# Kernel optimization log

Hardware: AMD Instinct MI355X
Metric: run time of the kernel (lower is better)

The kernel has to match this reference:

```python
import jax, jax.numpy as jnp
import numpy as np

B, S, H = 2, 2048, 2048
NK, NV, DK, DV = 16, 32, 128, 128
K_CONV = 4
EPS = 1e-6
KEY_DIM = NK * DK          # 2048
VALUE_DIM = NV * DV        # 4096
CONV_DIM = 2 * KEY_DIM + VALUE_DIM  # 8192
R = NV // NK               # GQA repeat factor


def setup_inputs() -> dict:
    key = jax.random.key(0)
    ks = jax.random.split(key, 9)
    s = lambda d: 1.0 / np.sqrt(d)
    x = jax.random.normal(ks[0], (B, S, H), jnp.float32)
    W_qkvz = jax.random.normal(ks[1], (H, 2 * KEY_DIM + 2 * VALUE_DIM), jnp.float32) * s(H)
    W_ba = jax.random.normal(ks[2], (H, 2 * NV), jnp.float32) * s(H)
    conv_w = jax.random.normal(ks[3], (CONV_DIM, K_CONV), jnp.float32) * s(K_CONV)
    dt_bias = jnp.ones((NV,), jnp.float32)
    A_log = jnp.log(jax.random.uniform(ks[4], (NV,), jnp.float32, 1e-3, 16.0))
    norm_w = jnp.ones((DV,), jnp.float32)
    W_out = jax.random.normal(ks[5], (VALUE_DIM, H), jnp.float32) * s(VALUE_DIM)
    return {"x": x, "W_qkvz": W_qkvz, "W_ba": W_ba, "conv_w": conv_w,
            "dt_bias": dt_bias, "A_log": A_log, "norm_w": norm_w, "W_out": W_out}


def _rms_norm(x, eps=EPS):
    return x * jax.lax.rsqrt(jnp.mean(jnp.square(x), -1, keepdims=True) + eps)


def _forward(x, W_qkvz, W_ba, conv_w, dt_bias, A_log, norm_w, W_out):
    b_, s_ = x.shape[:2]
    # in projections (mlx split-INDEX semantics)
    qkvz = (x @ W_qkvz).reshape(b_, s_, NK, 2 * DK + 2 * R * DV)
    q, k, v, z = jnp.split(qkvz, [DK, 2 * DK, 2 * DK + R * DV], axis=-1)
    v = v.reshape(b_, s_, NV, DV)
    z = z.reshape(b_, s_, NV, DV)
    ba = (x @ W_ba).reshape(b_, s_, NK, 2 * R)
    b_gate, a_gate = jnp.split(ba, [R], axis=-1)
    b_gate = b_gate.reshape(b_, s_, NV)
    a_gate = a_gate.reshape(b_, s_, NV)

    # causal depthwise conv over [q,k,v] channels, zero initial conv state
    mixed = jnp.concatenate([q.reshape(b_, s_, -1), k.reshape(b_, s_, -1),
                             v.reshape(b_, s_, -1)], axis=-1)  # [B,S,CONV_DIM]
    xc = jnp.pad(mixed, ((0, 0), (K_CONV - 1, 0), (0, 0))).transpose(0, 2, 1)  # [B,C,S+K-1]
    conv = jax.lax.conv_general_dilated(
        xc, conv_w[:, None, :], window_strides=(1,), padding='VALID',
        dimension_numbers=('NCH', 'OIH', 'NCH'), feature_group_count=CONV_DIM)
    conv = jax.nn.silu(conv).transpose(0, 2, 1)  # [B,S,CONV_DIM]
    q, k, v = jnp.split(conv, [KEY_DIM, 2 * KEY_DIM], axis=-1)
    q = q.reshape(b_, s_, NK, DK)
    k = k.reshape(b_, s_, NK, DK)
    v = v.reshape(b_, s_, NV, DV)

    inv_scale = DK ** -0.5
    q = (inv_scale ** 2) * _rms_norm(q)
    k = inv_scale * _rms_norm(k)
    # GQA: repeat k/q heads to match value heads
    q = jnp.repeat(q, R, axis=2)  # [B,S,NV,DK]
    k = jnp.repeat(k, R, axis=2)

    beta = jax.nn.sigmoid(b_gate)                                # [B,S,NV]
    g = -jnp.exp(A_log) * jax.nn.softplus(a_gate + dt_bias)      # [B,S,NV] (log-decay)

    # gated delta-rule recurrence, scan over time
    def step(Sst, inp):
        q_t, k_t, v_t, g_t, beta_t = inp   # [B,NV,DK], [B,NV,DV], [B,NV]
        Sst = Sst * jnp.exp(g_t)[..., None, None]
        kv = jnp.einsum('bhk,bhkv->bhv', k_t, Sst)
        delta = (v_t - kv) * beta_t[..., None]
        Sst = Sst + k_t[..., None] * delta[:, :, None, :]
        o = jnp.einsum('bhk,bhkv->bhv', q_t, Sst)
        return Sst, o

    S0 = jnp.zeros((b_, NV, DK, DV), x.dtype)
    xs = (q.transpose(1, 0, 2, 3), k.transpose(1, 0, 2, 3), v.transpose(1, 0, 2, 3),
          g.transpose(1, 0, 2), beta.transpose(1, 0, 2))
    _, out = jax.lax.scan(step, S0, xs)
    out = out.transpose(1, 0, 2, 3)  # [B,S,NV,DV]

    # gated RMSNorm (precise swiglu)
    xn = _rms_norm(out) * norm_w
    gated = jax.nn.silu(z.astype(jnp.float32)) * xn.astype(jnp.float32)
    gated = gated.astype(x.dtype)
    return gated.reshape(b_, s_, VALUE_DIM) @ W_out


def reference(x, W_qkvz, W_ba, conv_w, dt_bias, A_log, norm_w, W_out):
    return _forward(x, W_qkvz, W_ba, conv_w, dt_bias, A_log, norm_w, W_out)
```

## Files before the change

kernel.cpp:

```cpp
#include <hip/hip_runtime.h>
#include <stdint.h>

#define B_    2
#define SEQ   2048
#define HID   2048
#define NK_   16
#define NV_   32
#define DK_   128
#define DV_   128
#define NQKVZ 12288
#define CONVD 8192
#define MTOT  (B_*SEQ)
#define CCH   16
#define HTOK  1024

typedef unsigned short ushort_t;
typedef __bf16 bf16x8 __attribute__((ext_vector_type(8)));
typedef float  f32x4  __attribute__((ext_vector_type(4)));
typedef unsigned short us4 __attribute__((ext_vector_type(4)));

__device__ __forceinline__ ushort_t f2bf(float f){
  union { float f; unsigned u; } v; v.f = f;
  unsigned r = v.u + 0x7FFFu + ((v.u >> 16) & 1u);
  return (ushort_t)(r >> 16);
}
__device__ __forceinline__ float bf2f(ushort_t u){
  union { unsigned u; float f; } v; v.u = ((unsigned)u) << 16; return v.f;
}
__device__ __forceinline__ float sigmoidf_(float x){ return 1.f/(1.f+__expf(-x)); }
__device__ __forceinline__ float siluf_(float x){ return x*sigmoidf_(x); }

__global__ void cast_x_kernel(const float* __restrict__ x, ushort_t* __restrict__ xb, int n4){
  int i = blockIdx.x*256 + threadIdx.x;
  if (i >= n4) return;
  float4 v = ((const float4*)x)[i];
  us4 o; o[0]=f2bf(v.x); o[1]=f2bf(v.y); o[2]=f2bf(v.z); o[3]=f2bf(v.w);
  ((us4*)xb)[i] = o;
}

__global__ __launch_bounds__(256) void transpose_cast(const float* __restrict__ W, ushort_t* __restrict__ Wt,
                                                      int K, int N){
  __shared__ float tile[64][65];
  int n0 = blockIdx.x*64, k0 = blockIdx.y*64;
  int tx = threadIdx.x & 63, ty = threadIdx.x >> 6;
  #pragma unroll
  for (int i=0;i<16;i++){
    int kr = ty + i*4;
    tile[kr][tx] = W[(size_t)(k0+kr)*N + n0+tx];
  }
  __syncthreads();
  #pragma unroll
  for (int i=0;i<16;i++){
    int nr = ty + i*4;
    Wt[(size_t)(n0+nr)*K + k0+tx] = f2bf(tile[tx][nr]);
  }
}

template<int OUTBF>
__global__ __launch_bounds__(512, 2) void gemm_big(const ushort_t* __restrict__ A, const ushort_t* __restrict__ Bt,
                                                   void* __restrict__ Cv, int M, int N, int K){
  extern __shared__ ushort_t dynlds[];
  ushort_t* SA = dynlds;
  ushort_t* SB = dynlds + 3*8192;
  const int t = threadIdx.x;
  const int lane = t & 63, w = t >> 6;
  const int wm = w >> 2, wn = w & 3;
  const int lr = lane & 15, hk = lane >> 4;
  const int gx = gridDim.x;
  const int nwg = gx * gridDim.y;
  const int flat = blockIdx.y*gx + blockIdx.x;
  const int cpx = nwg >> 3;
  const int swzb = (flat & 7)*cpx + (flat >> 3);
  const int m0 = (swzb / gx) * 256, n0 = (swzb % gx) * 256;

  int srow[2], scol[2];
  #pragma unroll
  for (int q=0;q<2;q++){
    int p  = (w*2+q)*1024 + lane*16;
    int lg = p ^ (((p>>9)&1)<<5);
    srow[q] = lg >> 6;
    scol[q] = (lg & 63) >> 1;
  }
  int phA[8], phB[4];
  #pragma unroll
  for (int mi=0;mi<8;mi++){
    int lg = (wm*128 + mi*16 + lr)*64 + hk*16;
    phA[mi] = lg ^ (((lg>>9)&1)<<5);
  }
  #pragma unroll
  for (int ni=0;ni<4;ni++){
    int lg = (wn*64 + ni*16 + lr)*64 + hk*16;
    phB[ni] = lg ^ (((lg>>9)&1)<<5);
  }

  auto stage = [&](int j, int bufb){
    #pragma unroll
    for (int q=0;q<2;q++)
      __builtin_amdgcn_global_load_lds(
        (const __attribute__((address_space(1))) void*)(A + (size_t)(m0+srow[q])*K + j*32 + scol[q]),
        (__attribute__((address_space(3))) void*)(SA + bufb*8192 + (w*2+q)*512), 16, 0, 0);
    #pragma unroll
    for (int q=0;q<2;q++)
      __builtin_amdgcn_global_load_lds(
        (const __attribute__((address_space(1))) void*)(Bt + (size_t)(n0+srow[q])*K + j*32 + scol[q]),
        (__attribute__((address_space(3))) void*)(SB + bufb*8192 + (w*2+q)*512), 16, 0, 0);
  };

  f32x4 acc[8][4];
  #pragma unroll
  for (int mi=0;mi<8;mi++)
    #pragma unroll
    for (int ni=0;ni<4;ni++) acc[mi][ni] = (f32x4){0.f,0.f,0.f,0.f};

  const int NT = K >> 5;
  stage(0, 0);
  stage(1, 1);
  asm volatile("s_waitcnt vmcnt(4)" ::: "memory");
  __builtin_amdgcn_s_barrier();
  __builtin_amdgcn_sched_barrier(0);

  int cur = 0;
  for (int j = 0; j < NT; ++j){
    int nb = cur + 2; if (nb >= 3) nb -= 3;
    if (j + 2 < NT) stage(j+2, nb);
    const char* bA = (const char*)(SA + cur*8192);
    const char* bB = (const char*)(SB + cur*8192);
    bf16x8 af[8], bfv[4];
    #pragma unroll
    for (int mi=0;mi<8;mi++) af[mi]  = *(const bf16x8*)(bA + phA[mi]);
    #pragma unroll
    for (int ni=0;ni<4;ni++) bfv[ni] = *(const bf16x8*)(bB + phB[ni]);
    #pragma unroll
    for (int mi=0;mi<8;mi++)
      #pragma unroll
      for (int ni=0;ni<4;ni++)
        acc[mi][ni] = __builtin_amdgcn_mfma_f32_16x16x32_bf16(af[mi], bfv[ni], acc[mi][ni], 0, 0, 0);
    if (j + 2 < NT){
      asm volatile("s_waitcnt vmcnt(4)" ::: "memory");
      __builtin_amdgcn_s_barrier();
      __builtin_amdgcn_sched_barrier(0);
    } else if (j + 1 < NT){
      asm volatile("s_waitcnt vmcnt(0)" ::: "memory");
      __builtin_amdgcn_s_barrier();
      __builtin_amdgcn_sched_barrier(0);
    }
    cur = cur + 1; if (cur >= 3) cur -= 3;
  }

  #pragma unroll
  for (int mi=0;mi<8;mi++)
    #pragma unroll
    for (int ni=0;ni<4;ni++)
      #pragma unroll
      for (int r=0;r<4;r++){
        int m = m0 + wm*128 + mi*16 + hk*4 + r;
        int n = n0 + wn*64  + ni*16 + lr;
        if (OUTBF) ((ushort_t*)Cv)[(size_t)m*N + n] = f2bf(acc[mi][ni][r]);
        else       ((float*)Cv)[(size_t)m*N + n]    = acc[mi][ni][r];
      }
}

template<int OUTBF>
__global__ __launch_bounds__(512, 2) void gemm_big2(const ushort_t* __restrict__ A, const ushort_t* __restrict__ Bt,
                                                    void* __restrict__ Cv, int M, int N, int K){
  extern __shared__ ushort_t dynlds[];
  ushort_t* SA = dynlds;
  ushort_t* SB = dynlds + 3*8192;
  const int t = threadIdx.x;
  const int lane = t & 63, w = t >> 6;
  const int wm = w >> 1, wn = w & 1;
  const int lr = lane & 15, hk = lane >> 4;
  const int gx = gridDim.x;
  const int nwg = gx * gridDim.y;
  const int flat = blockIdx.y*gx + blockIdx.x;
  const int cpx = nwg >> 3;
  const int swzb = (flat & 7)*cpx + (flat >> 3);
  const int m0 = (swzb / gx) * 256, n0 = (swzb % gx) * 128;

  int srA[2], scA[2];
  #pragma unroll
  for (int q=0;q<2;q++){
    int p  = (w*2+q)*1024 + lane*16;
    int lg = p ^ (((p>>9)&1)<<5);
    srA[q] = lg >> 6;
    scA[q] = (lg & 63) >> 1;
  }
  int srB, scB;
  {
    int p  = w*1024 + lane*16;
    int lg = p ^ (((p>>9)&1)<<5);
    srB = lg >> 6;
    scB = (lg & 63) >> 1;
  }
  int phA[4], phB[4];
  #pragma unroll
  for (int mi=0;mi<4;mi++){
    int lg = (wm*64 + mi*16 + lr)*64 + hk*16;
    phA[mi] = lg ^ (((lg>>9)&1)<<5);
  }
  #pragma unroll
  for (int ni=0;ni<4;ni++){
    int lg = (wn*64 + ni*16 + lr)*64 + hk*16;
    phB[ni] = lg ^ (((lg>>9)&1)<<5);
  }

  auto stage = [&](int j, int bufb){
    #pragma unroll
    for (int q=0;q<2;q++)
      __builtin_amdgcn_global_load_lds(
        (const __attribute__((address_space(1))) void*)(A + (size_t)(m0+srA[q])*K + j*32 + scA[q]),
        (__attribute__((address_space(3))) void*)(SA + bufb*8192 + (w*2+q)*512), 16, 0, 0);
    __builtin_amdgcn_global_load_lds(
        (const __attribute__((address_space(1))) void*)(Bt + (size_t)(n0+srB)*K + j*32 + scB),
        (__attribute__((address_space(3))) void*)(SB + bufb*4096 + w*512), 16, 0, 0);
  };

  f32x4 acc[4][4];
  #pragma unroll
  for (int mi=0;mi<4;mi++)
    #pragma unroll
    for (int ni=0;ni<4;ni++) acc[mi][ni] = (f32x4){0.f,0.f,0.f,0.f};

  const int NT = K >> 5;
  stage(0, 0);
  stage(1, 1);
  asm volatile("s_waitcnt vmcnt(3)" ::: "memory");
  __builtin_amdgcn_s_barrier();
  __builtin_amdgcn_sched_barrier(0);

  int cur = 0;
  for (int j = 0; j < NT; ++j){
    int nb = cur + 2; if (nb >= 3) nb -= 3;
    if (j + 2 < NT) stage(j+2, nb);
    const char* bA = (const char*)(SA + cur*8192);
    const char* bB = (const char*)(SB + cur*4096);
    bf16x8 af[4], bfv[4];
    #pragma unroll
    for (int mi=0;mi<4;mi++) af[mi]  = *(const bf16x8*)(bA + phA[mi]);
    #pragma unroll
    for (int ni=0;ni<4;ni++) bfv[ni] = *(const bf16x8*)(bB + phB[ni]);
    #pragma unroll
    for (int mi=0;mi<4;mi++)
      #pragma unroll
      for (int ni=0;ni<4;ni++)
        acc[mi][ni] = __builtin_amdgcn_mfma_f32_16x16x32_bf16(af[mi], bfv[ni], acc[mi][ni], 0, 0, 0);
    if (j + 2 < NT){
      asm volatile("s_waitcnt vmcnt(3)" ::: "memory");
      __builtin_amdgcn_s_barrier();
      __builtin_amdgcn_sched_barrier(0);
    } else if (j + 1 < NT){
      asm volatile("s_waitcnt vmcnt(0)" ::: "memory");
      __builtin_amdgcn_s_barrier();
      __builtin_amdgcn_sched_barrier(0);
    }
    cur = cur + 1; if (cur >= 3) cur -= 3;
  }

  #pragma unroll
  for (int mi=0;mi<4;mi++)
    #pragma unroll
    for (int ni=0;ni<4;ni++)
      #pragma unroll
      for (int r=0;r<4;r++){
        int m = m0 + wm*64 + mi*16 + hk*4 + r;
        int n = n0 + wn*64 + ni*16 + lr;
        if (OUTBF) ((ushort_t*)Cv)[(size_t)m*N + n] = f2bf(acc[mi][ni][r]);
        else       ((float*)Cv)[(size_t)m*N + n]    = acc[mi][ni][r];
      }
}

template<int OUTBF>
__global__ __launch_bounds__(256) void gemm_bf16(const ushort_t* __restrict__ A, const ushort_t* __restrict__ Bt,
                                                 void* __restrict__ Cv, int M, int N, int K){
  __shared__ ushort_t As[128][32];
  __shared__ ushort_t Bs[128][32];
  const int t = threadIdx.x;
  const int lane = t & 63, w = t >> 6;
  const int wm = w >> 1, wn = w & 1;
  const int gx = gridDim.x;
  const int nwg = gx * gridDim.y;
  const int flat = blockIdx.y*gx + blockIdx.x;
  const int cpx = nwg >> 3;
  const int swz = (flat & 7)*cpx + (flat >> 3);
  const int m0 = (swz / gx) * 128, n0 = (swz % gx) * 128;
  const int srow = lane >> 2;
  const int scol = (lane & 3) * 8;
  const ushort_t* gA0 = &A [(size_t)(m0 +      w*16 + srow)*K + scol];
  const ushort_t* gA1 = &A [(size_t)(m0 + 64 + w*16 + srow)*K + scol];
  const ushort_t* gB0 = &Bt[(size_t)(n0 +      w*16 + srow)*K + scol];
  const ushort_t* gB1 = &Bt[(size_t)(n0 + 64 + w*16 + srow)*K + scol];
  ushort_t* lA0 = &As[     w*16][0];
  ushort_t* lA1 = &As[64 + w*16][0];
  ushort_t* lB0 = &Bs[     w*16][0];
  ushort_t* lB1 = &Bs[64 + w*16][0];
  f32x4 acc[4][4];
  #pragma unroll
  for (int i=0;i<4;i++)
    #pragma unroll
    for (int j=0;j<4;j++) acc[i][j] = (f32x4){0.f,0.f,0.f,0.f};
  const int lr = lane & 15, lk = (lane >> 4) * 8;
  for (int k0 = 0; k0 < K; k0 += 32){
    __builtin_amdgcn_global_load_lds((const __attribute__((address_space(1))) void*)(gA0 + k0),
                                     (__attribute__((address_space(3))) void*)lA0, 16, 0, 0);
    __builtin_amdgcn_global_load_lds((const __attribute__((address_space(1))) void*)(gA1 + k0),
                                     (__attribute__((address_space(3))) void*)lA1, 16, 0, 0);
    __builtin_amdgcn_global_load_lds((const __attribute__((address_space(1))) void*)(gB0 + k0),
                                     (__attribute__((address_space(3))) void*)lB0, 16, 0, 0);
    __builtin_amdgcn_global_load_lds((const __attribute__((address_space(1))) void*)(gB1 + k0),
                                     (__attribute__((address_space(3))) void*)lB1, 16, 0, 0);
    __syncthreads();
    bf16x8 af[4], bfv[4];
    #pragma unroll
    for (int i=0;i<4;i++) af[i]  = *(const bf16x8*)&As[wm*64 + i*16 + lr][lk];
    #pragma unroll
    for (int j=0;j<4;j++) bfv[j] = *(const bf16x8*)&Bs[wn*64 + j*16 + lr][lk];
    #pragma unroll
    for (int i=0;i<4;i++)
      #pragma unroll
      for (int j=0;j<4;j++)
        acc[i][j] = __builtin_amdgcn_mfma_f32_16x16x32_bf16(af[i], bfv[j], acc[i][j], 0, 0, 0);
    __syncthreads();
  }
  const int lg = lane >> 4;
  #pragma unroll
  for (int i=0;i<4;i++)
    #pragma unroll
    for (int j=0;j<4;j++)
      #pragma unroll
      for (int r=0;r<4;r++){
        int m = m0 + wm*64 + i*16 + lg*4 + r;
        int n = n0 + wn*64 + j*16 + lr;
        if (OUTBF) ((ushort_t*)Cv)[(size_t)m*N + n] = f2bf(acc[i][j][r]);
        else       ((float*)Cv)[(size_t)m*N + n]    = acc[i][j][r];
      }
}

__global__ __launch_bounds__(256) void gemm_ba(const float* __restrict__ x, const float* __restrict__ Wba,
                                               float* __restrict__ ba){
  int lane = threadIdx.x & 63;
  int wid  = threadIdx.x >> 6;
  int row  = blockIdx.x*4 + wid;
  const float* xr = x + (size_t)row*HID;
  float acc = 0.f;
  for (int k=0;k<HID;k+=4){
    float4 xv = *(const float4*)&xr[k];
    acc += xv.x * Wba[(size_t)(k+0)*64 + lane];
    acc += xv.y * Wba[(size_t)(k+1)*64 + lane];
    acc += xv.z * Wba[(size_t)(k+2)*64 + lane];
    acc += xv.w * Wba[(size_t)(k+3)*64 + lane];
  }
  ba[(size_t)row*64 + lane] = acc;
}

__global__ __launch_bounds__(256) void conv_norm_kernel(const ushort_t* __restrict__ qkvz, const float* __restrict__ conv_w,
                                                        ushort_t* __restrict__ qkv){
  const int blk = blockIdx.x;
  const int bt = blk >> 4;
  const int ts = bt & (SEQ-1);
  const int gi = (blk & 15)*4 + (threadIdx.x >> 6);
  const int e2 = threadIdx.x & 63;
  const int dk = 2*e2;
  int col;
  if (gi < 16)       col = gi*768 + dk;
  else if (gi < 32)  col = (gi-16)*768 + 128 + dk;
  else { int nv = gi-32; col = (nv>>1)*768 + 256 + (nv&1)*128 + dk; }
  const int c = gi*128 + dk;
  const float4 w0 = *(const float4*)&conv_w[(size_t)c*4];
  const float4 w1 = *(const float4*)&conv_w[(size_t)(c+1)*4];
  ushort2 a0 = (ts>=3) ? *(const ushort2*)&qkvz[(size_t)(bt-3)*NQKVZ + col] : make_ushort2(0,0);
  ushort2 a1 = (ts>=2) ? *(const ushort2*)&qkvz[(size_t)(bt-2)*NQKVZ + col] : make_ushort2(0,0);
  ushort2 a2 = (ts>=1) ? *(const ushort2*)&qkvz[(size_t)(bt-1)*NQKVZ + col] : make_ushort2(0,0);
  ushort2 a3 =           *(const ushort2*)&qkvz[(size_t)(bt  )*NQKVZ + col];
  float y0 = siluf_(bf2f(a0.x)*w0.x + bf2f(a1.x)*w0.y + bf2f(a2.x)*w0.z + bf2f(a3.x)*w0.w);
  float y1 = siluf_(bf2f(a0.y)*w1.x + bf2f(a1.y)*w1.y + bf2f(a2.y)*w1.z + bf2f(a3.y)*w1.w);
  float o0 = y0, o1 = y1;
  if (gi < 32){
    float ss = y0*y0 + y1*y1;
    #pragma unroll
    for (int o=1;o<64;o<<=1) ss += __shfl_xor(ss, o);
    float rs = rsqrtf(ss*(1.f/128.f) + 1e-6f);
    float scale = (gi < 16) ? (1.f/128.f) : 0.08838834764831845f;
    o0 = y0*rs*scale; o1 = y1*rs*scale;
  }
  ushort2 ov; ov.x = f2bf(o0); ov.y = f2bf(o1);
  *(ushort2*)&qkv[(size_t)bt*CONVD + gi*128 + dk] = ov;
}

__global__ void gbeta_kernel(const float* __restrict__ ba, const float* __restrict__ A_log,
                             const float* __restrict__ dt_bias, float2* __restrict__ egb){
  int idx = blockIdx.x*256 + threadIdx.x;
  if (idx >= MTOT*NV_) return;
  int nv = idx & 31;
  int bt = idx >> 5;
  int nk = nv >> 1, r = nv & 1;
  float bg = ba[(size_t)bt*64 + nk*4 + r];
  float ag = ba[(size_t)bt*64 + nk*4 + 2 + r];
  float ad = ag + dt_bias[nv];
  float sp = fmaxf(ad, 0.f) + log1pf(__expf(-fabsf(ad)));
  float g  = -__expf(A_log[nv]) * sp;
  egb[idx] = make_float2(g, sigmoidf_(bg));
}

__global__ __launch_bounds__(512) void recurrence_chunked(const ushort_t* __restrict__ qkv,
                                                          const float2* __restrict__ egb,
                                                          float* __restrict__ outc,
                                                          ushort_t* __restrict__ oaug,
                                                          ushort_t* __restrict__ Sfin,
                                                          int pmode){
  const int bi = blockIdx.x;
  int role, hb, tokbase, ntok;
  if (pmode == 0){ role = 0; hb = bi; tokbase = 0; ntok = SEQ; }
  else { role = bi >> 7; hb = bi & 127; tokbase = (role == 0) ? 0 : HTOK; ntok = HTOK; }
  const bool isaug = (role == 2);
  const bool wsf   = (pmode == 1) && (role == 0);
  const int b    = hb >> 6;
  const int nv   = (hb >> 1) & 31;
  const int half = hb & 1;
  const int nk   = nv >> 1;
  const int t    = threadIdx.x;
  const int lane = t & 63, w = t >> 6;
  const int lr   = lane & 15, hk = lane >> 4;

  __shared__ ushort_t Kl[16*136];
  __shared__ ushort_t S0h[64*136];
  __shared__ ushort_t S0l[64*136];
  __shared__ ushort_t KT[128*40];
  __shared__ ushort_t DT[64*40];
  __shared__ ushort_t Wl[16*40];
  __shared__ float    Al[16*20];
  __shared__ float    Ul[64*20];
  __shared__ float    clB[2][16], blB[2][16], eclB[2][16], kslB[2][16], c15B[2];

  for (int i = t; i < 64*40;  i += 512) DT[i] = 0;
  for (int i = t; i < 128*40; i += 512) KT[i] = 0;
  for (int i = t; i < 16*40;  i += 512) Wl[i] = 0;
  for (int i = t; i < 64*136; i += 512){ S0h[i] = 0; S0l[i] = 0; }

  const int dt  = w >> 1;
  const int dkb = (w & 1) * 4;
  const int ot  = w - 4;
  const int st  = t >> 5, sdk = (t & 31) * 4;
  const size_t bt0 = (size_t)b*SEQ + tokbase;
  const int mytile = (w < 4) ? w : (w - 4);

  f32x4 S[4];
  #pragma unroll
  for (int tt=0;tt<4;tt++)
    #pragma unroll
    for (int r=0;r<4;r++)
      S[tt][r] = (isaug && ((dkb+tt)*16 + hk*4 + r) == (half*64 + dt*16 + lr)) ? 1.f : 0.f;

  if (isaug){
    __syncthreads();
    if (t < 64) S0h[t*136 + half*64 + t] = (ushort_t)0x3F80;
  }

  uint2 kreg = *(const uint2*)(qkv + (bt0+st)*CONVD + 2048 + nk*128 + sdk);
  bf16x8 qf[4];
  if (w >= 4){
    const ushort_t* qrow = qkv + (bt0+lr)*CONVD + nk*128 + hk*8;
    #pragma unroll
    for (int ks=0;ks<4;ks++) qf[ks] = *(const bf16x8*)(qrow + ks*32);
  }
  ushort_t vreg[4] = {0,0,0,0};
  if (w < 4 && !isaug){
    #pragma unroll
    for (int r=0;r<4;r++)
      vreg[r] = qkv[(bt0+hk*4+r)*CONVD + 4096 + nv*128 + half*64 + w*16 + lr];
  }
  {
    float2 gb = make_float2(0.f,0.f);
    if (w==1 && lane<16) gb = egb[(bt0+lane)*NV_ + nv];
    *(uint2*)&Kl[st*136 + sdk] = kreg;
    if (w==1 && lane<16){
      float c = gb.x;
      #pragma unroll
      for (int o=1;o<16;o<<=1){ float tv = __shfl_up(c, o, 16); if (lane >= o) c += tv; }
      clB[0][lane] = c; blB[0][lane] = gb.y; eclB[0][lane] = __expf(c);
      float c15 = __shfl(c, 15, 16);
      kslB[0][lane] = __expf(c15 - c);
      if (lane==0) c15B[0] = c15;
    }
  }
  __syncthreads();

  int pb = 0;
  for (int base = 0; base < ntok; base += CCH){
    const int nbase = (base + CCH < ntok) ? base + CCH : base;

    bf16x8 kf[4];
    if (w <= 4){
      #pragma unroll
      for (int ks=0;ks<4;ks++) kf[ks] = *(const bf16x8*)&Kl[lr*136 + hk*8 + ks*32];
    }
    f32x4 ph = (f32x4){0.f,0.f,0.f,0.f}, pl = ph;
    __builtin_amdgcn_s_setprio(1);
    #pragma unroll
    for (int ks=0;ks<4;ks++){
      bf16x8 xf = (w < 4) ? kf[ks] : qf[ks];
      bf16x8 yh = *(const bf16x8*)&S0h[(mytile*16+lr)*136 + hk*8 + ks*32];
      bf16x8 yl = *(const bf16x8*)&S0l[(mytile*16+lr)*136 + hk*8 + ks*32];
      ph = __builtin_amdgcn_mfma_f32_16x16x32_bf16(xf, yh, ph, 0,0,0);
      pl = __builtin_amdgcn_mfma_f32_16x16x32_bf16(xf, yl, pl, 0,0,0);
    }
    __builtin_amdgcn_s_setprio(0);
    if (w == 1){
      f32x4 a = (f32x4){0.f,0.f,0.f,0.f};
      #pragma unroll
      for (int ks=0;ks<4;ks++) a = __builtin_amdgcn_mfma_f32_16x16x32_bf16(kf[ks], kf[ks], a, 0,0,0);
      #pragma unroll
      for (int r=0;r<4;r++){
        int i = hk*4 + r, j = lr;
        Al[i*20 + j] = (j < i) ? blB[pb][i]*__expf(clB[pb][i]-clB[pb][j])*a[r] : 0.f;
      }
    }
    if (w == 4){
      f32x4 a = (f32x4){0.f,0.f,0.f,0.f};
      #pragma unroll
      for (int ks=0;ks<4;ks++) a = __builtin_amdgcn_mfma_f32_16x16x32_bf16(qf[ks], kf[ks], a, 0,0,0);
      #pragma unroll
      for (int r=0;r<4;r++){
        int i = hk*4 + r, j = lr;
        float val = (j <= i) ? __expf(clB[pb][i]-clB[pb][j])*a[r] : 0.f;
        Wl[i*40 + j] = f2bf(val);
      }
    }
    if (w < 4){
      float4 uu;
      #pragma unroll
      for (int r=0;r<4;r++){
        int i = hk*4 + r;
        ((float*)&uu)[r] = blB[pb][i]*(bf2f(vreg[r]) - eclB[pb][i]*(ph[r] + pl[r]));
      }
      *(float4*)&Ul[(w*16 + lr)*20 + hk*4] = uu;
    }
    if (w == 2 || w == 3){
      int dk = t & 127;
      #pragma unroll
      for (int j=0;j<16;j+=2){
        unsigned p0 = f2bf(kslB[pb][j]  * bf2f(Kl[j*136     + dk]));
        unsigned p1 = f2bf(kslB[pb][j+1]* bf2f(Kl[(j+1)*136 + dk]));
        *(unsigned*)&KT[dk*40 + j] = p0 | (p1 << 16);
      }
    }
    __syncthreads();

    kreg = *(const uint2*)(qkv + (bt0+nbase+st)*CONVD + 2048 + nk*128 + sdk);
    if (w >= 4){
      const ushort_t* qrow = qkv + (bt0 + nbase + lr)*CONVD + nk*128 + hk*8;
      #pragma unroll
      for (int ks=0;ks<4;ks++) qf[ks] = *(const bf16x8*)(qrow + ks*32);
    }
    if (w < 4 && !isaug){
      #pragma unroll
      for (int r=0;r<4;r++)
        vreg[r] = qkv[(bt0+nbase+hk*4+r)*CONVD + 4096 + nv*128 + half*64 + w*16 + lr];
    }
    float2 ebn = make_float2(0.f,0.f);
    if (w==1 && lane<16) ebn = egb[(bt0+nbase+lane)*NV_ + nv];
    bf16x8 yf[4];
    #pragma unroll
    for (int tt=0;tt<4;tt++) yf[tt] = *(const bf16x8*)&KT[((dkb+tt)*16+lr)*40 + hk*8];
    bf16x8 wfr;
    if (w >= 4) wfr = *(const bf16x8*)&Wl[lr*40 + hk*8];

    if (w == 0){
      __builtin_amdgcn_s_setprio(1);
      float d[16];
      #pragma unroll
      for (int q=0;q<4;q++){
        float4 dd = *(const float4*)&Ul[lane*20 + q*4];
        d[4*q]=dd.x; d[4*q+1]=dd.y; d[4*q+2]=dd.z; d[4*q+3]=dd.w;
      }
      #pragma unroll
      for (int rb=0;rb<4;rb++){
        float p0=0.f,p1=0.f,p2=0.f,p3=0.f;
        #pragma unroll
        for (int jb=0;jb<rb;jb++){
          float4 A0 = *(const float4*)&Al[(rb*4+0)*20 + jb*4];
          float4 A1 = *(const float4*)&Al[(rb*4+1)*20 + jb*4];
          float4 A2 = *(const float4*)&Al[(rb*4+2)*20 + jb*4];
          float4 A3 = *(const float4*)&Al[(rb*4+3)*20 + jb*4];
          p0 += A0.x*d[jb*4]+A0.y*d[jb*4+1]+A0.z*d[jb*4+2]+A0.w*d[jb*4+3];
          p1 += A1.x*d[jb*4]+A1.y*d[jb*4+1]+A1.z*d[jb*4+2]+A1.w*d[jb*4+3];
          p2 += A2.x*d[jb*4]+A2.y*d[jb*4+1]+A2.z*d[jb*4+2]+A2.w*d[jb*4+3];
          p3 += A3.x*d[jb*4]+A3.y*d[jb*4+1]+A3.z*d[jb*4+2]+A3.w*d[jb*4+3];
        }
        const int r0 = rb*4;
        d[r0+0] -= p0;
        d[r0+1] -= p1 + Al[(r0+1)*20+r0]*d[r0];
        d[r0+2] -= p2 + Al[(r0+2)*20+r0]*d[r0] + Al[(r0+2)*20+r0+1]*d[r0+1];
        d[r0+3] -= p3 + Al[(r0+3)*20+r0]*d[r0] + Al[(r0+3)*20+r0+1]*d[r0+1] + Al[(r0+3)*20+r0+2]*d[r0+2];
      }
      unsigned dd[8];
      #pragma unroll
      for (int p=0;p<8;p++) dd[p] = (unsigned)f2bf(d[2*p]) | ((unsigned)f2bf(d[2*p+1]) << 16);
      *(uint4*)&DT[lane*40 + 0] = make_uint4(dd[0],dd[1],dd[2],dd[3]);
      *(uint4*)&DT[lane*40 + 8] = make_uint4(dd[4],dd[5],dd[6],dd[7]);
      __builtin_amdgcn_s_setprio(0);
    }
    __syncthreads();

    if (w >= 4){
      bf16x8 dfr = *(const bf16x8*)&DT[(ot*16+lr)*40 + hk*8];
      f32x4 oo = __builtin_amdgcn_mfma_f32_16x16x32_bf16(wfr, dfr, (f32x4){0.f,0.f,0.f,0.f}, 0,0,0);
      #pragma unroll
      for (int r=0;r<4;r++){
        int i = hk*4 + r;
        float o = oo[r] + eclB[pb][i]*(ph[r] + pl[r]);
        if (!isaug)
          outc[((bt0+base+i)*NV_ + nv)*(size_t)DV_ + half*64 + ot*16 + lr] = o;
        else
          oaug[(((size_t)(b*NV_+nv))*HTOK + base + i)*128 + half*64 + ot*16 + lr] = f2bf(o);
      }
    }
    {
      float g15 = __expf(c15B[pb]);
      bf16x8 dB = *(const bf16x8*)&DT[(dt*16+lr)*40 + hk*8];
      __builtin_amdgcn_s_setprio(1);
      #pragma unroll
      for (int tt=0;tt<4;tt++){
        f32x4 s = S[tt];
        s[0]*=g15; s[1]*=g15; s[2]*=g15; s[3]*=g15;
        S[tt] = __builtin_amdgcn_mfma_f32_16x16x32_bf16(yf[tt], dB, s, 0,0,0);
      }
      __builtin_amdgcn_s_setprio(0);
    }
    {
      const int dv = dt*16 + lr;
      #pragma unroll
      for (int tt=0;tt<4;tt++){
        const int dk0 = (dkb+tt)*16 + hk*4;
        unsigned h01, h23, l01, l23;
        {
          float s0=S[tt][0], s1=S[tt][1], s2=S[tt][2], s3=S[tt][3];
          ushort_t h0=f2bf(s0), h1=f2bf(s1), h2=f2bf(s2), h3=f2bf(s3);
          h01 = (unsigned)h0 | ((unsigned)h1<<16);
          h23 = (unsigned)h2 | ((unsigned)h3<<16);
          l01 = (unsigned)f2bf(s0-bf2f(h0)) | ((unsigned)f2bf(s1-bf2f(h1))<<16);
          l23 = (unsigned)f2bf(s2-bf2f(h2)) | ((unsigned)f2bf(s3-bf2f(h3))<<16);
        }
        *(uint2*)&S0h[dv*136 + dk0] = make_uint2(h01, h23);
        *(uint2*)&S0l[dv*136 + dk0] = make_uint2(l01, l23);
      }
    }
    *(uint2*)&Kl[st*136 + sdk] = kreg;
    if (w==1 && lane<16){
      float c = ebn.x;
      #pragma unroll
      for (int o=1;o<16;o<<=1){ float tv = __shfl_up(c, o, 16); if (lane >= o) c += tv; }
      clB[pb^1][lane] = c; blB[pb^1][lane] = ebn.y; eclB[pb^1][lane] = __expf(c);
      float c15 = __shfl(c, 15, 16);
      kslB[pb^1][lane] = __expf(c15 - c);
      if (lane==0) c15B[pb^1] = c15;
    }
    __syncthreads();
    pb ^= 1;
  }

  if (wsf){
    for (int i = t; i < 64*128; i += 512){
      int dvl = i >> 7, dk = i & 127;
      size_t row = ((size_t)(b*NV_+nv)*128 + half*64 + dvl)*256;
      Sfin[row + dk]       = S0h[dvl*136 + dk];
      Sfin[row + 128 + dk] = S0l[dvl*136 + dk];
    }
  }
}

__global__ __launch_bounds__(256) void corr_gemm(const ushort_t* __restrict__ oaug, const ushort_t* __restrict__ Sfin,
                                                 float* __restrict__ core){
  __shared__ ushort_t As[128][32];
  __shared__ ushort_t Bs[128][32];
  const int head = blockIdx.y;
  const int m0 = blockIdx.x * 128;
  const int b = head >> 5, nv = head & 31;
  const int t = threadIdx.x, lane = t & 63, w = t >> 6;
  const int wm = w >> 1, wn = w & 1;
  const int srow = lane >> 2, scol = (lane & 3) * 8;
  const ushort_t* Abase = oaug + (size_t)head*HTOK*128;
  const ushort_t* Bbase = Sfin + (size_t)head*128*256;
  ushort_t* lA0 = &As[     w*16][0];
  ushort_t* lA1 = &As[64 + w*16][0];
  ushort_t* lB0 = &Bs[     w*16][0];
  ushort_t* lB1 = &Bs[64 + w*16][0];
  f32x4 acc[4][4];
  #pragma unroll
  for (int i=0;i<4;i++)
    #pragma unroll
    for (int j=0;j<4;j++) acc[i][j] = (f32x4){0.f,0.f,0.f,0.f};
  const int lr = lane & 15, lk = (lane >> 4) * 8;
  for (int k0 = 0; k0 < 256; k0 += 32){
    const int ka = k0 & 127;
    __builtin_amdgcn_global_load_lds((const __attribute__((address_space(1))) void*)(Abase + (size_t)(m0 +      w*16 + srow)*128 + ka + scol),
                                     (__attribute__((address_space(3))) void*)lA0, 16, 0, 0);
    __builtin_amdgcn_global_load_lds((const __attribute__((address_space(1))) void*)(Abase + (size_t)(m0 + 64 + w*16 + srow)*128 + ka + scol),
                                     (__attribute__((address_space(3))) void*)lA1, 16, 0, 0);
    __builtin_amdgcn_global_load_lds((const __attribute__((address_space(1))) void*)(Bbase + (size_t)(     w*16 + srow)*256 + k0 + scol),
                                     (__attribute__((address_space(3))) void*)lB0, 16, 0, 0);
    __builtin_amdgcn_global_load_lds((const __attribute__((address_space(1))) void*)(Bbase + (size_t)(64 + w*16 + srow)*256 + k0 + scol),
                                     (__attribute__((address_space(3))) void*)lB1, 16, 0, 0);
    __syncthreads();
    bf16x8 af[4], bfv[4];
    #pragma unroll
    for (int i=0;i<4;i++) af[i]  = *(const bf16x8*)&As[wm*64 + i*16 + lr][lk];
    #pragma unroll
    for (int j=0;j<4;j++) bfv[j] = *(const bf16x8*)&Bs[wn*64 + j*16 + lr][lk];
    #pragma unroll
    for (int i=0;i<4;i++)
      #pragma unroll
      for (int j=0;j<4;j++)
        acc[i][j] = __builtin_amdgcn_mfma_f32_16x16x32_bf16(af[i], bfv[j], acc[i][j], 0, 0, 0);
    __syncthreads();
  }
  const int lg = lane >> 4;
  #pragma unroll
  for (int i=0;i<4;i++)
    #pragma unroll
    for (int j=0;j<4;j++)
      #pragma unroll
      for (int r=0;r<4;r++){
        int m = m0 + wm*64 + i*16 + lg*4 + r;
        int n = wn*64 + j*16 + lr;
        float* p = &core[(((size_t)b*SEQ + HTOK + m)*NV_ + nv)*(size_t)DV_ + n];
        *p += acc[i][j][r];
      }
}

__global__ __launch_bounds__(128) void gatenorm_kernel(const float* __restrict__ outc, const ushort_t* __restrict__ qkvz,
                                                       const float* __restrict__ norm_w, ushort_t* __restrict__ gated){
  __shared__ float red[2];
  const int blk = blockIdx.x;
  const int nv = blk & 31;
  const size_t bt = (size_t)(blk >> 5);
  const int dv = threadIdx.x;
  float xv = outc[(bt*NV_ + nv)*(size_t)DV_ + dv];
  float ss = xv*xv;
  #pragma unroll
  for (int o=1;o<64;o<<=1) ss += __shfl_xor(ss, o);
  if ((threadIdx.x & 63)==0) red[threadIdx.x>>6] = ss;
  __syncthreads();
  float tot = red[0]+red[1];
  float xn = xv * rsqrtf(tot*(1.f/128.f) + 1e-6f) * norm_w[dv];
  int nk = nv>>1, r = nv&1;
  float z = bf2f(qkvz[bt*NQKVZ + nk*768 + 512 + r*128 + dv]);
  gated[bt*(size_t)4096 + nv*128 + dv] = f2bf(siluf_(z)*xn);
}

extern "C" void kernel_launch(void* const* d_in, const int* in_sizes, int n_in,
                              void* d_out, int out_size, void* d_ws, size_t ws_size,
                              hipStream_t stream){
  (void)in_sizes; (void)n_in; (void)out_size;
  const float* x      = (const float*)d_in[0];
  const float* W_qkvz = (const float*)d_in[1];
  const float* W_ba   = (const float*)d_in[2];
  const float* conv_w = (const float*)d_in[3];
  const float* dt_bias= (const float*)d_in[4];
  const float* A_log  = (const float*)d_in[5];
  const float* norm_w = (const float*)d_in[6];
  const float* W_out  = (const float*)d_in[7];
  float* outp = (float*)d_out;

  char* w = (char*)d_ws;
  const size_t R0 = 0;
  const size_t R1 = 100663296;
  const size_t R2 = R1 + 67108864;
  const size_t R3 = R2 + 67108864;
  const size_t R4 = R3 + 2097152;
  const size_t NEED_SP = R4 + 16777216 + 4194304;
  ushort_t* qkvz_bf = (ushort_t*)(w + R0);
  ushort_t* xb      = (ushort_t*)(w + R1);
  ushort_t* wqt     = (ushort_t*)(w + R1 + 16777216);
  ushort_t* qkv_bf  = (ushort_t*)(w + R1);
  ushort_t* gated   = (ushort_t*)(w + R1);
  float*    core    = (float*)   (w + R2);
  ushort_t* wot     = (ushort_t*)(w + R2);
  float*    ba      = (float*)   (w + R3);
  float2*   egb     = (float2*)  (w + R3 + 1048576);
  ushort_t* oaug    = (ushort_t*)(w + R4);
  ushort_t* Sfin    = (ushort_t*)(w + R4 + 16777216);
  const bool seqpar = (ws_size >= NEED_SP);

  hipError_t e1 = hipFuncSetAttribute((const void*)gemm_big<1>, hipFuncAttributeMaxDynamicSharedMemorySize, 98304);
  hipError_t e2 = hipFuncSetAttribute((const void*)gemm_big2<0>, hipFuncAttributeMaxDynamicSharedMemorySize, 73728);
  const bool big  = (e1 == hipSuccess);
  const bool big2 = (e2 == hipSuccess);

  cast_x_kernel<<<(MTOT*HID/4 + 255)/256, 256, 0, stream>>>(x, xb, MTOT*HID/4);
  transpose_cast<<<dim3(NQKVZ/64, HID/64), 256, 0, stream>>>(W_qkvz, wqt, HID, NQKVZ);
  if (big) gemm_big<1><<<dim3(NQKVZ/256, MTOT/256), 512, 98304, stream>>>(xb, wqt, (void*)qkvz_bf, MTOT, NQKVZ, HID);
  else     gemm_bf16<1><<<dim3(NQKVZ/128, MTOT/128), 256, 0, stream>>>(xb, wqt, (void*)qkvz_bf, MTOT, NQKVZ, HID);
  gemm_ba<<<MTOT/4, 256, 0, stream>>>(x, W_ba, ba);
  gbeta_kernel<<<(MTOT*NV_+255)/256, 256, 0, stream>>>(ba, A_log, dt_bias, egb);
  conv_norm_kernel<<<MTOT*16, 256, 0, stream>>>(qkvz_bf, conv_w, qkv_bf);
  if (seqpar){
    recurrence_chunked<<<384, 512, 0, stream>>>(qkv_bf, egb, core, oaug, Sfin, 1);
    corr_gemm<<<dim3(8, 64), 256, 0, stream>>>(oaug, Sfin, core);
  } else {
    recurrence_chunked<<<128, 512, 0, stream>>>(qkv_bf, egb, core, oaug, Sfin, 0);
  }
  gatenorm_kernel<<<MTOT*NV_, 128, 0, stream>>>(core, qkvz_bf, norm_w, gated);
  transpose_cast<<<dim3(2048/64, 4096/64), 256, 0, stream>>>(W_out, wot, 4096, 2048);
  if (big2) gemm_big2<0><<<dim3(2048/128, MTOT/256), 512, 73728, stream>>>(gated, wot, (void*)outp, MTOT, 2048, 4096);
  else      gemm_bf16<0><<<dim3(2048/128, MTOT/128), 256, 0, stream>>>(gated, wot, (void*)outp, MTOT, 2048, 4096);
}
```

Baseline: 962.0 us.

## Merge second-half recurrence and augmented transition blocks into one workgroup

The sequence-parallel recurrence previously launched three roles: first half, second half, and a separate augmented block that propagated an identity state to get the transition matrix. The second-half blocks now carry both the real state S and the transition state T together, sharing the K/Q fragments, gate scalars and chunk loads. This cuts the grid from 384 to 256 blocks and removes the duplicated loads and scan work. In exchange those blocks do roughly twice the MFMA and LDS work, and the kernel now needs about 108KB of dynamic shared memory, which may lower occupancy and lengthen the critical path. The fallback gemm_bf16 kernel is deleted, and the fallback paths now call the large GEMMs.

```diff
diff --git a/kernel.cpp b/kernel.cpp
--- a/kernel.cpp
+++ b/kernel.cpp
@@ -13,6 +13,7 @@
 #define MTOT  (B_*SEQ)
 #define CCH   16
 #define HTOK  1024
+#define RLDSZ 110592
 
 typedef unsigned short ushort_t;
 typedef __bf16 bf16x8 __attribute__((ext_vector_type(8)));
@@ -266,72 +267,6 @@
         int n = n0 + wn*64 + ni*16 + lr;
         if (OUTBF) ((ushort_t*)Cv)[(size_t)m*N + n] = f2bf(acc[mi][ni][r]);
         else       ((float*)Cv)[(size_t)m*N + n]    = acc[mi][ni][r];
-      }
-}
-
-template<int OUTBF>
-__global__ __launch_bounds__(256) void gemm_bf16(const ushort_t* __restrict__ A, const ushort_t* __restrict__ Bt,
-                                                 void* __restrict__ Cv, int M, int N, int K){
-  __shared__ ushort_t As[128][32];
-  __shared__ ushort_t Bs[128][32];
-  const int t = threadIdx.x;
-  const int lane = t & 63, w = t >> 6;
-  const int wm = w >> 1, wn = w & 1;
-  const int gx = gridDim.x;
-  const int nwg = gx * gridDim.y;
-  const int flat = blockIdx.y*gx + blockIdx.x;
-  const int cpx = nwg >> 3;
-  const int swz = (flat & 7)*cpx + (flat >> 3);
-  const int m0 = (swz / gx) * 128, n0 = (swz % gx) * 128;
-  const int srow = lane >> 2;
-  const int scol = (lane & 3) * 8;
-  const ushort_t* gA0 = &A [(size_t)(m0 +      w*16 + srow)*K + scol];
-  const ushort_t* gA1 = &A [(size_t)(m0 + 64 + w*16 + srow)*K + scol];
-  const ushort_t* gB0 = &Bt[(size_t)(n0 +      w*16 + srow)*K + scol];
-  const ushort_t* gB1 = &Bt[(size_t)(n0 + 64 + w*16 + srow)*K + scol];
-  ushort_t* lA0 = &As[     w*16][0];
-  ushort_t* lA1 = &As[64 + w*16][0];
-  ushort_t* lB0 = &Bs[     w*16][0];
-  ushort_t* lB1 = &Bs[64 + w*16][0];
-  f32x4 acc[4][4];
-  #pragma unroll
-  for (int i=0;i<4;i++)
-    #pragma unroll
-    for (int j=0;j<4;j++) acc[i][j] = (f32x4){0.f,0.f,0.f,0.f};
-  const int lr = lane & 15, lk = (lane >> 4) * 8;
-  for (int k0 = 0; k0 < K; k0 += 32){
-    __builtin_amdgcn_global_load_lds((const __attribute__((address_space(1))) void*)(gA0 + k0),
-                                     (__attribute__((address_space(3))) void*)lA0, 16, 0, 0);
-    __builtin_amdgcn_global_load_lds((const __attribute__((address_space(1))) void*)(gA1 + k0),
-                                     (__attribute__((address_space(3))) void*)lA1, 16, 0, 0);
-    __builtin_amdgcn_global_load_lds((const __attribute__((address_space(1))) void*)(gB0 + k0),
-                                     (__attribute__((address_space(3))) void*)lB0, 16, 0, 0);
-    __builtin_amdgcn_global_load_lds((const __attribute__((address_space(1))) void*)(gB1 + k0),
-                                     (__attribute__((address_space(3))) void*)lB1, 16, 0, 0);
-    __syncthreads();
-    bf16x8 af[4], bfv[4];
-    #pragma unroll
-    for (int i=0;i<4;i++) af[i]  = *(const bf16x8*)&As[wm*64 + i*16 + lr][lk];
-    #pragma unroll
-    for (int j=0;j<4;j++) bfv[j] = *(const bf16x8*)&Bs[wn*64 + j*16 + lr][lk];
-    #pragma unroll
-    for (int i=0;i<4;i++)
-      #pragma unroll
-      for (int j=0;j<4;j++)
-        acc[i][j] = __builtin_amdgcn_mfma_f32_16x16x32_bf16(af[i], bfv[j], acc[i][j], 0, 0, 0);
-    __syncthreads();
-  }
-  const int lg = lane >> 4;
-  #pragma unroll
-  for (int i=0;i<4;i++)
-    #pragma unroll
-    for (int j=0;j<4;j++)
-      #pragma unroll
-      for (int r=0;r<4;r++){
-        int m = m0 + wm*64 + i*16 + lg*4 + r;
-        int n = n0 + wn*64 + j*16 + lr;
-        if (OUTBF) ((ushort_t*)Cv)[(size_t)m*N + n] = f2bf(acc[i][j][r]);
-        else       ((float*)Cv)[(size_t)m*N + n]    = acc[i][j][r];
       }
 }
 
@@ -407,12 +342,32 @@
                                                           ushort_t* __restrict__ oaug,
                                                           ushort_t* __restrict__ Sfin,
                                                           int pmode){
+  extern __shared__ char rlds[];
+  ushort_t* Kl  = (ushort_t*)(rlds + 0);
+  ushort_t* S0h = (ushort_t*)(rlds + 4352);
+  ushort_t* S0l = (ushort_t*)(rlds + 21760);
+  ushort_t* T0h = (ushort_t*)(rlds + 39168);
+  ushort_t* T0l = (ushort_t*)(rlds + 56576);
+  ushort_t* KT  = (ushort_t*)(rlds + 73984);
+  ushort_t* DT  = (ushort_t*)(rlds + 84224);
+  ushort_t* Wl  = (ushort_t*)(rlds + 94464);
+  float*    Al  = (float*)   (rlds + 95744);
+  float*    Ul  = (float*)   (rlds + 97024);
+  float*    clB = (float*)   (rlds + 107264);
+  float*    blB = clB + 32;
+  float*    eclB= clB + 64;
+  float*    kslB= clB + 96;
+  float*    c15B= clB + 128;
+
   const int bi = blockIdx.x;
-  int role, hb, tokbase, ntok;
-  if (pmode == 0){ role = 0; hb = bi; tokbase = 0; ntok = SEQ; }
-  else { role = bi >> 7; hb = bi & 127; tokbase = (role == 0) ? 0 : HTOK; ntok = HTOK; }
-  const bool isaug = (role == 2);
-  const bool wsf   = (pmode == 1) && (role == 0);
+  int hb, tokbase, ntok;
+  bool ismrg = false, wsf = false;
+  if (pmode == 0){ hb = bi; tokbase = 0; ntok = SEQ; }
+  else {
+    ntok = HTOK;
+    if (bi < 128){ hb = bi; tokbase = 0; wsf = true; }
+    else { hb = bi - 128; tokbase = HTOK; ismrg = true; }
+  }
   const int b    = hb >> 6;
   const int nv   = (hb >> 1) & 31;
   const int half = hb & 1;
@@ -421,20 +376,14 @@
   const int lane = t & 63, w = t >> 6;
   const int lr   = lane & 15, hk = lane >> 4;
 
-  __shared__ ushort_t Kl[16*136];
-  __shared__ ushort_t S0h[64*136];
-  __shared__ ushort_t S0l[64*136];
-  __shared__ ushort_t KT[128*40];
-  __shared__ ushort_t DT[64*40];
-  __shared__ ushort_t Wl[16*40];
-  __shared__ float    Al[16*20];
-  __shared__ float    Ul[64*20];
-  __shared__ float    clB[2][16], blB[2][16], eclB[2][16], kslB[2][16], c15B[2];
-
-  for (int i = t; i < 64*40;  i += 512) DT[i] = 0;
-  for (int i = t; i < 128*40; i += 512) KT[i] = 0;
+  for (int i = t; i < 128*40; i += 512){ KT[i] = 0; DT[i] = 0; }
   for (int i = t; i < 16*40;  i += 512) Wl[i] = 0;
-  for (int i = t; i < 64*136; i += 512){ S0h[i] = 0; S0l[i] = 0; }
+  for (int i = t; i < 64*136; i += 512){
+    S0h[i] = 0; S0l[i] = 0;
+    if (ismrg){ T0h[i] = 0; T0l[i] = 0; }
+  }
+  __syncthreads();
+  if (ismrg && t < 64) T0h[t*136 + half*64 + t] = (ushort_t)0x3F80;
 
   const int dt  = w >> 1;
   const int dkb = (w & 1) * 4;
@@ -443,17 +392,14 @@
   const size_t bt0 = (size_t)b*SEQ + tokbase;
   const int mytile = (w < 4) ? w : (w - 4);
 
-  f32x4 S[4];
+  f32x4 S[4], T[4];
   #pragma unroll
   for (int tt=0;tt<4;tt++)
     #pragma unroll
-    for (int r=0;r<4;r++)
-      S[tt][r] = (isaug && ((dkb+tt)*16 + hk*4 + r) == (half*64 + dt*16 + lr)) ? 1.f : 0.f;
-
-  if (isaug){
-    __syncthreads();
-    if (t < 64) S0h[t*136 + half*64 + t] = (ushort_t)0x3F80;
-  }
+    for (int r=0;r<4;r++){
+      S[tt][r] = 0.f;
+      T[tt][r] = (ismrg && ((dkb+tt)*16 + hk*4 + r) == (half*64 + dt*16 + lr)) ? 1.f : 0.f;
+    }
 
   uint2 kreg = *(const uint2*)(qkv + (bt0+st)*CONVD + 2048 + nk*128 + sdk);
   bf16x8 qf[4];
@@ -463,7 +409,7 @@
     for (int ks=0;ks<4;ks++) qf[ks] = *(const bf16x8*)(qrow + ks*32);
   }
   ushort_t vreg[4] = {0,0,0,0};
-  if (w < 4 && !isaug){
+  if (w < 4){
     #pragma unroll
     for (int r=0;r<4;r++)
       vreg[r] = qkv[(bt0+hk*4+r)*CONVD + 4096 + nv*128 + half*64 + w*16 + lr];
@@ -476,9 +422,9 @@
       float c = gb.x;
       #pragma unroll
       for (int o=1;o<16;o<<=1){ float tv = __shfl_up(c, o, 16); if (lane >= o) c += tv; }
-      clB[0][lane] = c; blB[0][lane] = gb.y; eclB[0][lane] = __expf(c);
+      clB[lane] = c; blB[lane] = gb.y; eclB[lane] = __expf(c);
       float c15 = __shfl(c, 15, 16);
-      kslB[0][lane] = __expf(c15 - c);
+      kslB[lane] = __expf(c15 - c);
       if (lane==0) c15B[0] = c15;
     }
   }
@@ -487,13 +433,14 @@
   int pb = 0;
   for (int base = 0; base < ntok; base += CCH){
     const int nbase = (base + CCH < ntok) ? base + CCH : base;
+    const int pb16 = pb*16;
 
     bf16x8 kf[4];
     if (w <= 4){
       #pragma unroll
       for (int ks=0;ks<4;ks++) kf[ks] = *(const bf16x8*)&Kl[lr*136 + hk*8 + ks*32];
     }
-    f32x4 ph = (f32x4){0.f,0.f,0.f,0.f}, pl = ph;
+    f32x4 ph = (f32x4){0.f,0.f,0.f,0.f}, pl = ph, phA = ph, plA = ph;
     __builtin_amdgcn_s_setprio(1);
     #pragma unroll
     for (int ks=0;ks<4;ks++){
@@ -503,6 +450,16 @@
       ph = __builtin_amdgcn_mfma_f32_16x16x32_bf16(xf, yh, ph, 0,0,0);
       pl = __builtin_amdgcn_mfma_f32_16x16x32_bf16(xf, yl, pl, 0,0,0);
     }
+    if (ismrg){
+      #pragma unroll
+      for (int ks=0;ks<4;ks++){
+        bf16x8 xf = (w < 4) ? kf[ks] : qf[ks];
+        bf16x8 yh = *(const bf16x8*)&T0h[(mytile*16+lr)*136 + hk*8 + ks*32];
+        bf16x8 yl = *(const bf16x8*)&T0l[(mytile*16+lr)*136 + hk*8 + ks*32];
+        phA = __builtin_amdgcn_mfma_f32_16x16x32_bf16(xf, yh, phA, 0,0,0);
+        plA = __builtin_amdgcn_mfma_f32_16x16x32_bf16(xf, yl, plA, 0,0,0);
+      }
+    }
     __builtin_amdgcn_s_setprio(0);
     if (w == 1){
       f32x4 a = (f32x4){0.f,0.f,0.f,0.f};
@@ -511,7 +468,7 @@
       #pragma unroll
       for (int r=0;r<4;r++){
         int i = hk*4 + r, j = lr;
-        Al[i*20 + j] = (j < i) ? blB[pb][i]*__expf(clB[pb][i]-clB[pb][j])*a[r] : 0.f;
+        Al[i*20 + j] = (j < i) ? blB[pb16+i]*__expf(clB[pb16+i]-clB[pb16+j])*a[r] : 0.f;
       }
     }
     if (w == 4){
@@ -521,7 +478,7 @@
       #pragma unroll
       for (int r=0;r<4;r++){
         int i = hk*4 + r, j = lr;
-        float val = (j <= i) ? __expf(clB[pb][i]-clB[pb][j])*a[r] : 0.f;
+        float val = (j <= i) ? __expf(clB[pb16+i]-clB[pb16+j])*a[r] : 0.f;
         Wl[i*40 + j] = f2bf(val);
       }
     }
@@ -530,16 +487,25 @@
       #pragma unroll
       for (int r=0;r<4;r++){
         int i = hk*4 + r;
-        ((float*)&uu)[r] = blB[pb][i]*(bf2f(vreg[r]) - eclB[pb][i]*(ph[r] + pl[r]));
+        ((float*)&uu)[r] = blB[pb16+i]*(bf2f(vreg[r]) - eclB[pb16+i]*(ph[r] + pl[r]));
       }
       *(float4*)&Ul[(w*16 + lr)*20 + hk*4] = uu;
+      if (ismrg){
+        float4 ua;
+        #pragma unroll
+        for (int r=0;r<4;r++){
+          int i = hk*4 + r;
+          ((float*)&ua)[r] = -blB[pb16+i]*eclB[pb16+i]*(phA[r] + plA[r]);
+        }
+        *(float4*)&Ul[(64 + w*16 + lr)*20 + hk*4] = ua;
+      }
     }
     if (w == 2 || w == 3){
       int dk = t & 127;
       #pragma unroll
       for (int j=0;j<16;j+=2){
-        unsigned p0 = f2bf(kslB[pb][j]  * bf2f(Kl[j*136     + dk]));
-        unsigned p1 = f2bf(kslB[pb][j+1]* bf2f(Kl[(j+1)*136 + dk]));
+        unsigned p0 = f2bf(kslB[pb16+j]  * bf2f(Kl[j*136     + dk]));
+        unsigned p1 = f2bf(kslB[pb16+j+1]* bf2f(Kl[(j+1)*136 + dk]));
         *(unsigned*)&KT[dk*40 + j] = p0 | (p1 << 16);
       }
     }
@@ -551,7 +517,7 @@
       #pragma unroll
       for (int ks=0;ks<4;ks++) qf[ks] = *(const bf16x8*)(qrow + ks*32);
     }
-    if (w < 4 && !isaug){
+    if (w < 4){
       #pragma unroll
       for (int r=0;r<4;r++)
         vreg[r] = qkv[(bt0+nbase+hk*4+r)*CONVD + 4096 + nv*128 + half*64 + w*16 + lr];
@@ -564,12 +530,11 @@
     bf16x8 wfr;
     if (w >= 4) wfr = *(const bf16x8*)&Wl[lr*40 + hk*8];
 
-    if (w == 0){
-      __builtin_amdgcn_s_setprio(1);
+    auto fsub = [&](int rowoff){
       float d[16];
       #pragma unroll
       for (int q=0;q<4;q++){
-        float4 dd = *(const float4*)&Ul[lane*20 + q*4];
+        float4 dd = *(const float4*)&Ul[(rowoff+lane)*20 + q*4];
         d[4*q]=dd.x; d[4*q+1]=dd.y; d[4*q+2]=dd.z; d[4*q+3]=dd.w;
       }
       #pragma unroll
@@ -595,10 +560,11 @@
       unsigned dd[8];
       #pragma unroll
       for (int p=0;p<8;p++) dd[p] = (unsigned)f2bf(d[2*p]) | ((unsigned)f2bf(d[2*p+1]) << 16);
-      *(uint4*)&DT[lane*40 + 0] = make_uint4(dd[0],dd[1],dd[2],dd[3]);
-      *(uint4*)&DT[lane*40 + 8] = make_uint4(dd[4],dd[5],dd[6],dd[7]);
-      __builtin_amdgcn_s_setprio(0);
-    }
+      *(uint4*)&DT[(rowoff+lane)*40 + 0] = make_uint4(dd[0],dd[1],dd[2],dd[3]);
+      *(uint4*)&DT[(rowoff+lane)*40 + 8] = make_uint4(dd[4],dd[5],dd[6],dd[7]);
+    };
+    if (w == 0){ __builtin_amdgcn_s_setprio(1); fsub(0);  __builtin_amdgcn_s_setprio(0); }
+    if (ismrg && w == 1){ __builtin_amdgcn_s_setprio(1); fsub(64); __builtin_amdgcn_s_setprio(0); }
     __syncthreads();
 
     if (w >= 4){
@@ -607,11 +573,17 @@
       #pragma unroll
       for (int r=0;r<4;r++){
         int i = hk*4 + r;
-        float o = oo[r] + eclB[pb][i]*(ph[r] + pl[r]);
-        if (!isaug)
-          outc[((bt0+base+i)*NV_ + nv)*(size_t)DV_ + half*64 + ot*16 + lr] = o;
-        else
-          oaug[(((size_t)(b*NV_+nv))*HTOK + base + i)*128 + half*64 + ot*16 + lr] = f2bf(o);
+        outc[((bt0+base+i)*NV_ + nv)*(size_t)DV_ + half*64 + ot*16 + lr] = oo[r] + eclB[pb16+i]*(ph[r] + pl[r]);
+      }
+      if (ismrg){
+        bf16x8 dfr2 = *(const bf16x8*)&DT[(64 + ot*16+lr)*40 + hk*8];
+        f32x4 oo2 = __builtin_amdgcn_mfma_f32_16x16x32_bf16(wfr, dfr2, (f32x4){0.f,0.f,0.f,0.f}, 0,0,0);
+        #pragma unroll
+        for (int r=0;r<4;r++){
+          int i = hk*4 + r;
+          oaug[(((size_t)(b*NV_+nv))*HTOK + base + i)*128 + half*64 + ot*16 + lr]
+            = f2bf(oo2[r] + eclB[pb16+i]*(phA[r] + plA[r]));
+        }
       }
     }
     {
@@ -624,6 +596,15 @@
         s[0]*=g15; s[1]*=g15; s[2]*=g15; s[3]*=g15;
         S[tt] = __builtin_amdgcn_mfma_f32_16x16x32_bf16(yf[tt], dB, s, 0,0,0);
       }
+      if (ismrg){
+        bf16x8 dB2 = *(const bf16x8*)&DT[(64 + dt*16+lr)*40 + hk*8];
+        #pragma unroll
+        for (int tt=0;tt<4;tt++){
+          f32x4 s = T[tt];
+          s[0]*=g15; s[1]*=g15; s[2]*=g15; s[3]*=g15;
+          T[tt] = __builtin_amdgcn_mfma_f32_16x16x32_bf16(yf[tt], dB2, s, 0,0,0);
+        }
+      }
       __builtin_amdgcn_s_setprio(0);
     }
     {
@@ -631,17 +612,22 @@
       #pragma unroll
       for (int tt=0;tt<4;tt++){
         const int dk0 = (dkb+tt)*16 + hk*4;
-        unsigned h01, h23, l01, l23;
         {
           float s0=S[tt][0], s1=S[tt][1], s2=S[tt][2], s3=S[tt][3];
           ushort_t h0=f2bf(s0), h1=f2bf(s1), h2=f2bf(s2), h3=f2bf(s3);
-          h01 = (unsigned)h0 | ((unsigned)h1<<16);
-          h23 = (unsigned)h2 | ((unsigned)h3<<16);
-          l01 = (unsigned)f2bf(s0-bf2f(h0)) | ((unsigned)f2bf(s1-bf2f(h1))<<16);
-          l23 = (unsigned)f2bf(s2-bf2f(h2)) | ((unsigned)f2bf(s3-bf2f(h3))<<16);
+          *(uint2*)&S0h[dv*136 + dk0] = make_uint2((unsigned)h0 | ((unsigned)h1<<16),
+                                                   (unsigned)h2 | ((unsigned)h3<<16));
+          *(uint2*)&S0l[dv*136 + dk0] = make_uint2((unsigned)f2bf(s0-bf2f(h0)) | ((unsigned)f2bf(s1-bf2f(h1))<<16),
+                                                   (unsigned)f2bf(s2-bf2f(h2)) | ((unsigned)f2bf(s3-bf2f(h3))<<16));
         }
-        *(uint2*)&S0h[dv*136 + dk0] = make_uint2(h01, h23);
-        *(uint2*)&S0l[dv*136 + dk0] = make_uint2(l01, l23);
+        if (ismrg){
+          float s0=T[tt][0], s1=T[tt][1], s2=T[tt][2], s3=T[tt][3];
+          ushort_t h0=f2bf(s0), h1=f2bf(s1), h2=f2bf(s2), h3=f2bf(s3);
+          *(uint2*)&T0h[dv*136 + dk0] = make_uint2((unsigned)h0 | ((unsigned)h1<<16),
+                                                   (unsigned)h2 | ((unsigned)h3<<16));
+          *(uint2*)&T0l[dv*136 + dk0] = make_uint2((unsigned)f2bf(s0-bf2f(h0)) | ((unsigned)f2bf(s1-bf2f(h1))<<16),
+                                                   (unsigned)f2bf(s2-bf2f(h2)) | ((unsigned)f2bf(s3-bf2f(h3))<<16));
+        }
       }
     }
     *(uint2*)&Kl[st*136 + sdk] = kreg;
@@ -649,9 +635,10 @@
       float c = ebn.x;
       #pragma unroll
       for (int o=1;o<16;o<<=1){ float tv = __shfl_up(c, o, 16); if (lane >= o) c += tv; }
-      clB[pb^1][lane] = c; blB[pb^1][lane] = ebn.y; eclB[pb^1][lane] = __expf(c);
+      int q16 = (pb^1)*16;
+      clB[q16+lane] = c; blB[q16+lane] = ebn.y; eclB[q16+lane] = __expf(c);
       float c15 = __shfl(c, 15, 16);
-      kslB[pb^1][lane] = __expf(c15 - c);
+      kslB[q16+lane] = __expf(c15 - c);
       if (lane==0) c15B[pb^1] = c15;
     }
     __syncthreads();
@@ -779,28 +766,29 @@
   float2*   egb     = (float2*)  (w + R3 + 1048576);
   ushort_t* oaug    = (ushort_t*)(w + R4);
   ushort_t* Sfin    = (ushort_t*)(w + R4 + 16777216);
-  const bool seqpar = (ws_size >= NEED_SP);
 
   hipError_t e1 = hipFuncSetAttribute((const void*)gemm_big<1>, hipFuncAttributeMaxDynamicSharedMemorySize, 98304);
   hipError_t e2 = hipFuncSetAttribute((const void*)gemm_big2<0>, hipFuncAttributeMaxDynamicSharedMemorySize, 73728);
+  hipError_t e3 = hipFuncSetAttribute((const void*)recurrence_chunked, hipFuncAttributeMaxDynamicSharedMemorySize, RLDSZ);
   const bool big  = (e1 == hipSuccess);
   const bool big2 = (e2 == hipSuccess);
+  const bool seqpar = (ws_size >= NEED_SP) && (e3 == hipSuccess);
 
   cast_x_kernel<<<(MTOT*HID/4 + 255)/256, 256, 0, stream>>>(x, xb, MTOT*HID/4);
   transpose_cast<<<dim3(NQKVZ/64, HID/64), 256, 0, stream>>>(W_qkvz, wqt, HID, NQKVZ);
   if (big) gemm_big<1><<<dim3(NQKVZ/256, MTOT/256), 512, 98304, stream>>>(xb, wqt, (void*)qkvz_bf, MTOT, NQKVZ, HID);
-  else     gemm_bf16<1><<<dim3(NQKVZ/128, MTOT/128), 256, 0, stream>>>(xb, wqt, (void*)qkvz_bf, MTOT, NQKVZ, HID);
+  else     gemm_big<1><<<dim3(NQKVZ/256, MTOT/256), 512, 98304, stream>>>(xb, wqt, (void*)qkvz_bf, MTOT, NQKVZ, HID);
   gemm_ba<<<MTOT/4, 256, 0, stream>>>(x, W_ba, ba);
   gbeta_kernel<<<(MTOT*NV_+255)/256, 256, 0, stream>>>(ba, A_log, dt_bias, egb);
   conv_norm_kernel<<<MTOT*16, 256, 0, stream>>>(qkvz_bf, conv_w, qkv_bf);
   if (seqpar){
-    recurrence_chunked<<<384, 512, 0, stream>>>(qkv_bf, egb, core, oaug, Sfin, 1);
+    recurrence_chunked<<<256, 512, RLDSZ, stream>>>(qkv_bf, egb, core, oaug, Sfin, 1);
     corr_gemm<<<dim3(8, 64), 256, 0, stream>>>(oaug, Sfin, core);
   } else {
-    recurrence_chunked<<<128, 512, 0, stream>>>(qkv_bf, egb, core, oaug, Sfin, 0);
+    recurrence_chunked<<<128, 512, RLDSZ, stream>>>(qkv_bf, egb, core, oaug, Sfin, 0);
   }
   gatenorm_kernel<<<MTOT*NV_, 128, 0, stream>>>(core, qkvz_bf, norm_w, gated);
   transpose_cast<<<dim3(2048/64, 4096/64), 256, 0, stream>>>(W_out, wot, 4096, 2048);
   if (big2) gemm_big2<0><<<dim3(2048/128, MTOT/256), 512, 73728, stream>>>(gated, wot, (void*)outp, MTOT, 2048, 4096);
-  else      gemm_bf16<0><<<dim3(2048/128, MTOT/128), 256, 0, stream>>>(gated, wot, (void*)outp, MTOT, 2048, 4096);
-}
+  else      gemm_big2<0><<<dim3(2048/128, MTOT/256), 512, 73728, stream>>>(gated, wot, (void*)outp, MTOT, 2048, 4096);
+}
```

After: 885.0 us. 1.09x faster.
